# Optimization experiments

Measured on AMD Instinct MI355X. Metric: run time of the kernel, lower is better.

## Reference

```python
import jax, jax.numpy as jnp
import numpy as np

ENC_HID = 512
DEC_HID = 512


def setup_inputs() -> dict:
    key = jax.random.key(0)
    k1, k2, k3, k4, k5 = jax.random.split(key, 5)
    hidden = jax.random.normal(k1, (64, DEC_HID), dtype=jnp.float32)
    encoder_outputs = jax.random.normal(k2, (1024, 64, 2 * ENC_HID), dtype=jnp.float32)
    in_dim = 2 * ENC_HID + DEC_HID
    # Linear params (stored as [in, out] for x @ W + b)
    scale = 1.0 / np.sqrt(in_dim)
    W = jax.random.uniform(k3, (in_dim, DEC_HID), dtype=jnp.float32, minval=-scale, maxval=scale)
    b = jax.random.uniform(k4, (DEC_HID,), dtype=jnp.float32, minval=-scale, maxval=scale)
    v = jax.random.uniform(k5, (DEC_HID,), dtype=jnp.float32)  # torch.rand in [0,1)
    return {"hidden": hidden, "encoder_outputs": encoder_outputs, "W": W, "b": b, "v": v}


def reference(hidden, encoder_outputs, W, b, v):
    # hidden: [B, Dd]; encoder_outputs: [S, B, 2*De]
    src_len = encoder_outputs.shape[0]
    enc = jnp.transpose(encoder_outputs, (1, 0, 2))            # [B, S, 2*De]
    hid = jnp.broadcast_to(hidden[:, None, :], (hidden.shape[0], src_len, hidden.shape[1]))  # [B, S, Dd]
    concat = jnp.concatenate([hid, enc], axis=2)               # [B, S, Dd+2*De]
    energy = jnp.tanh(concat @ W + b)                          # [B, S, Dd]
    scores = jnp.einsum("bsd,d->bs", energy, v)                # [B, S]
    return jax.nn.softmax(scores, axis=1)
```

## Files before the change

### kernel.cpp

```cpp
#include <hip/hip_runtime.h>
#include <stdint.h>


typedef float  floatx4 __attribute__((ext_vector_type(4)));
typedef __bf16 bf16x8  __attribute__((ext_vector_type(8)));
typedef short  short8  __attribute__((ext_vector_type(8)));

union bfu { bf16x8 v; short8 s; };

#define LOG2E_X2 2.8853900817779268f

#define BAR()                                              \
  do {                                                     \
    asm volatile("s_waitcnt lgkmcnt(0)" ::: "memory");     \
    __builtin_amdgcn_sched_barrier(0);                     \
    __builtin_amdgcn_s_barrier();                          \
    __builtin_amdgcn_sched_barrier(0);                     \
  } while (0)

__global__ void wt_convert(const float* __restrict__ W, __bf16* __restrict__ Bp) {
  __shared__ float tile[64][65];
  const int kt = blockIdx.x >> 3;
  const int nt = blockIdx.x & 7;
  const int c  = threadIdx.x & 63;
  const int r4 = threadIdx.x >> 6;
  #pragma unroll 4
  for (int i = 0; i < 16; i++) {
    int r = i * 4 + r4;
    tile[r][c] = W[(long)(512 + kt * 64 + r) * 512 + nt * 64 + c];
  }
  __syncthreads();
  const int n_loc = threadIdx.x & 63;
  const int kc4   = threadIdx.x >> 6;
  const int n_g   = nt * 64 + n_loc;
  const int wv    = n_g >> 7;
  const int ct    = (n_g >> 4) & 7;
  const int t     = n_g & 15;
  #pragma unroll
  for (int i = 0; i < 2; i++) {
    int chunk = i * 4 + kc4;
    int k_g   = kt * 64 + chunk * 8;
    int T     = k_g >> 5;
    int q     = (k_g >> 3) & 3;
    union bfu u;
    #pragma unroll
    for (int j = 0; j < 8; j++) u.v[j] = (__bf16)tile[chunk * 8 + j][n_loc];
    long cidx = ((long)(T * 4 + wv) * 8 + ct) * 64 + q * 16 + t;
    *(bf16x8*)(Bp + cidx * 8) = u.v;
  }
}

__global__ void hproj_kernel(const float* __restrict__ hidden,
                             const float* __restrict__ W,
                             const float* __restrict__ bias,
                             float* __restrict__ hproj) {
  const int tid = threadIdx.x;
  const int b_  = blockIdx.x >> 2;
  const int kc  = blockIdx.x & 3;
  __shared__ float hid[128];
  if (tid < 128) hid[tid] = hidden[b_ * 512 + kc * 128 + tid];
  __syncthreads();
  float acc = (kc == 0) ? bias[tid] : 0.f;
  const float* Wp = W + (long)(kc * 128) * 512 + tid;
  #pragma unroll 8
  for (int k = 0; k < 128; k++) acc = fmaf(hid[k], Wp[(long)k * 512], acc);
  atomicAdd(&hproj[b_ * 512 + tid], acc);
}

__global__ __launch_bounds__(256, 2) void gemm_score(
    const float* __restrict__ enc,
    const __bf16* __restrict__ Bp,
    const float* __restrict__ hproj,
    const float* __restrict__ v,
    float* __restrict__ scores)
{
  __shared__ __bf16 ldsA[2][2048];
  __shared__ float bscore[64];

  const int tid  = threadIdx.x;
  const int lane = tid & 63;
  const int wv   = tid >> 6;
  const int q    = lane >> 4;
  const int t    = lane & 15;
  const long m0  = (long)blockIdx.x * 64;

  const int sm = tid >> 2;
  const int sf = tid & 3;
  const float* ap = enc + (m0 + sm) * 1024 + sf * 8;
  __bf16* aw0 = &ldsA[0][sf * 512 + ((sm * 8) ^ (sf * 16))];
  __bf16* aw1 = &ldsA[1][sf * 512 + ((sm * 8) ^ (sf * 16))];

  const __bf16* ar0 = &ldsA[0][q * 512 + ((t * 8) ^ (q * 16))];
  const __bf16* ar1 = &ldsA[1][q * 512 + ((t * 8) ^ (q * 16))];

  const __bf16* bpb = Bp + ((long)wv * 512 + lane) * 8;

  if (tid < 64) bscore[tid] = 0.f;

  floatx4 acc[4][8];
  #pragma unroll
  for (int i = 0; i < 4; i++)
    #pragma unroll
    for (int j = 0; j < 8; j++)
      acc[i][j] = (floatx4){0.f, 0.f, 0.f, 0.f};

  floatx4 ra[3][2];
  short8  bfr[2][8];

  auto issueA = [&](int T, int s) {
    const float* p = ap + T * 32;
    ra[s][0] = *(const floatx4*)(p);
    ra[s][1] = *(const floatx4*)(p + 4);
  };
  auto writeA = [&](int s, __bf16* dst) {
    union bfu u;
    #pragma unroll
    for (int j = 0; j < 4; j++) {
      u.v[j]     = (__bf16)ra[s][0][j];
      u.v[4 + j] = (__bf16)ra[s][1][j];
    }
    *(bf16x8*)dst = u.v;
  };
  auto loadB = [&](int T, int s) {
    #pragma unroll
    for (int ct = 0; ct < 8; ct++) {
      union bfu u;
      u.v = *(const bf16x8*)(bpb + (long)T * 16384 + ct * 512);
      bfr[s][ct] = u.s;
    }
  };
  auto compute = [&](const __bf16* base, int bs) {
    #pragma unroll
    for (int rt = 0; rt < 4; rt++) {
      union bfu u;
      u.v = *(const bf16x8*)(base + rt * 128);
      #pragma unroll
      for (int ct = 0; ct < 8; ct++)
        acc[rt][ct] = __builtin_amdgcn_mfma_f32_16x16x32_bf16(
            u.s, bfr[bs][ct], acc[rt][ct], 0, 0, 0);
    }
  };

  issueA(0, 0); issueA(1, 1); issueA(2, 2);
  loadB(0, 0);  loadB(1, 1);
  writeA(0, aw0);
  BAR();

#define PHASE(T, SI, SW)                                   \
  {                                                        \
    if ((T) < 29) issueA((T) + 3, SI);                     \
    if ((T) < 31) writeA(SW, ((T) & 1) ? aw0 : aw1);       \
    compute(((T) & 1) ? ar1 : ar0, (T) & 1);               \
    if ((T) < 30) loadB((T) + 2, (T) & 1);                 \
    BAR();                                                 \
  }

  PHASE(0, 0, 1)  PHASE(1, 1, 2)  PHASE(2, 2, 0)  PHASE(3, 0, 1)
  PHASE(4, 1, 2)  PHASE(5, 2, 0)  PHASE(6, 0, 1)  PHASE(7, 1, 2)
  PHASE(8, 2, 0)  PHASE(9, 0, 1)  PHASE(10, 1, 2) PHASE(11, 2, 0)
  PHASE(12, 0, 1) PHASE(13, 1, 2) PHASE(14, 2, 0) PHASE(15, 0, 1)
  PHASE(16, 1, 2) PHASE(17, 2, 0) PHASE(18, 0, 1) PHASE(19, 1, 2)
  PHASE(20, 2, 0) PHASE(21, 0, 1) PHASE(22, 1, 2) PHASE(23, 2, 0)
  PHASE(24, 0, 1) PHASE(25, 1, 2) PHASE(26, 2, 0) PHASE(27, 0, 1)
  PHASE(28, 1, 2) PHASE(29, 2, 0) PHASE(30, 0, 1) PHASE(31, 1, 2)
#undef PHASE

  float vv[8];
  #pragma unroll
  for (int ct = 0; ct < 8; ct++) vv[ct] = v[wv * 128 + ct * 16 + t];

  #pragma unroll
  for (int rt = 0; rt < 4; rt++) {
    #pragma unroll
    for (int r = 0; r < 4; r++) {
      int row = rt * 16 + q * 4 + r;
      const float* hrow = hproj + row * 512 + wv * 128 + t;
      float s = 0.f;
      #pragma unroll
      for (int ct = 0; ct < 8; ct++) {
        float e  = acc[rt][ct][r] + hrow[ct * 16];
        float ex = __builtin_amdgcn_exp2f(e * LOG2E_X2);
        float th = 1.f - 2.f * __builtin_amdgcn_rcpf(ex + 1.f);
        s = fmaf(vv[ct], th, s);
      }
      s += __shfl_xor(s, 1);
      s += __shfl_xor(s, 2);
      s += __shfl_xor(s, 4);
      s += __shfl_xor(s, 8);
      if (t == 0) atomicAdd(&bscore[row], s);
    }
  }
  __syncthreads();
  if (tid < 64) scores[(long)tid * 1024 + blockIdx.x] = bscore[tid];
}

__global__ void softmax_kernel(const float* __restrict__ scores,
                               float* __restrict__ out) {
  const int b_   = blockIdx.x;
  const int tid  = threadIdx.x;
  const int lane = tid & 63;
  const int wv   = tid >> 6;
  __shared__ float redmax[4], redsum[4];

  float x[4];
  #pragma unroll
  for (int i = 0; i < 4; i++) x[i] = scores[b_ * 1024 + i * 256 + tid];
  float mx = fmaxf(fmaxf(x[0], x[1]), fmaxf(x[2], x[3]));
  #pragma unroll
  for (int off = 1; off < 64; off <<= 1) mx = fmaxf(mx, __shfl_xor(mx, off));
  if (lane == 0) redmax[wv] = mx;
  __syncthreads();
  mx = fmaxf(fmaxf(redmax[0], redmax[1]), fmaxf(redmax[2], redmax[3]));

  float e[4], s = 0.f;
  #pragma unroll
  for (int i = 0; i < 4; i++) { e[i] = __expf(x[i] - mx); s += e[i]; }
  #pragma unroll
  for (int off = 1; off < 64; off <<= 1) s += __shfl_xor(s, off);
  if (lane == 0) redsum[wv] = s;
  __syncthreads();
  s = redsum[0] + redsum[1] + redsum[2] + redsum[3];
  float inv = 1.f / s;
  #pragma unroll
  for (int i = 0; i < 4; i++) out[b_ * 1024 + i * 256 + tid] = e[i] * inv;
}

extern "C" void kernel_launch(void* const* d_in, const int* in_sizes, int n_in,
                              void* d_out, int out_size, void* d_ws, size_t ws_size,
                              hipStream_t stream) {
  (void)in_sizes; (void)n_in; (void)out_size; (void)ws_size;
  const float* hidden = (const float*)d_in[0];
  const float* enc    = (const float*)d_in[1];
  const float* W      = (const float*)d_in[2];
  const float* bias   = (const float*)d_in[3];
  const float* v      = (const float*)d_in[4];
  float* out = (float*)d_out;

  char* ws = (char*)d_ws;
  __bf16* Bp    = (__bf16*)ws;
  float*  hproj = (float*)(ws + (1 << 20));
  float*  scores= (float*)(ws + (1 << 20) + (128 << 10));

  hipMemsetAsync(hproj, 0, 64 * 512 * sizeof(float), stream);
  wt_convert<<<128, 256, 0, stream>>>(W, Bp);
  hproj_kernel<<<256, 512, 0, stream>>>(hidden, W, bias, hproj);
  gemm_score<<<1024, 256, 0, stream>>>(enc, Bp, hproj, v, scores);
  softmax_kernel<<<64, 256, 0, stream>>>(scores, out);
}
```

Before: 417.3 us.

## Split gemm_score tile across 8 waves and reorder loads after MFMA compute

Doubles the gemm_score block to 512 threads with waves arranged as a 2x4 grid over rows and columns. Each wave now holds half the accumulators (2x8 tiles instead of 4x8), which frees registers and raises occupancy. Each thread loads one float4 of the A tile per phase instead of two. Each phase is reordered so the MFMA compute runs first, followed by the LDS write and B loads, with the next global A load issued last and sched_barriers fencing the groups. Every wave now reloads the full B fragments, doubling B traffic per block through L2/L1.

```diff
diff --git a/kernel.cpp b/kernel.cpp
--- a/kernel.cpp
+++ b/kernel.cpp
@@ -3,10 +3,12 @@
 
 
 typedef float  floatx4 __attribute__((ext_vector_type(4)));
+typedef __bf16 bf16x4  __attribute__((ext_vector_type(4)));
 typedef __bf16 bf16x8  __attribute__((ext_vector_type(8)));
 typedef short  short8  __attribute__((ext_vector_type(8)));
 
-union bfu { bf16x8 v; short8 s; };
+union bfu  { bf16x8 v; short8 s; };
+union bfu4 { bf16x4 v; uint2 u; };
 
 #define LOG2E_X2 2.8853900817779268f
 
@@ -17,6 +19,8 @@
     __builtin_amdgcn_s_barrier();                          \
     __builtin_amdgcn_sched_barrier(0);                     \
   } while (0)
+
+#define SB() __builtin_amdgcn_sched_barrier(0)
 
 __global__ void wt_convert(const float* __restrict__ W, __bf16* __restrict__ Bp) {
   __shared__ float tile[64][65];
@@ -33,7 +37,7 @@
   const int n_loc = threadIdx.x & 63;
   const int kc4   = threadIdx.x >> 6;
   const int n_g   = nt * 64 + n_loc;
-  const int wv    = n_g >> 7;
+  const int wc    = n_g >> 7;
   const int ct    = (n_g >> 4) & 7;
   const int t     = n_g & 15;
   #pragma unroll
@@ -45,7 +49,7 @@
     union bfu u;
     #pragma unroll
     for (int j = 0; j < 8; j++) u.v[j] = (__bf16)tile[chunk * 8 + j][n_loc];
-    long cidx = ((long)(T * 4 + wv) * 8 + ct) * 64 + q * 16 + t;
+    long cidx = ((long)(T * 4 + wc) * 8 + ct) * 64 + q * 16 + t;
     *(bf16x8*)(Bp + cidx * 8) = u.v;
   }
 }
@@ -67,7 +71,7 @@
   atomicAdd(&hproj[b_ * 512 + tid], acc);
 }
 
-__global__ __launch_bounds__(256, 2) void gemm_score(
+__global__ __launch_bounds__(512, 4) void gemm_score(
     const float* __restrict__ enc,
     const __bf16* __restrict__ Bp,
     const float* __restrict__ hproj,
@@ -80,46 +84,42 @@
   const int tid  = threadIdx.x;
   const int lane = tid & 63;
   const int wv   = tid >> 6;
+  const int wc   = wv & 3;
+  const int wr   = wv >> 2;
   const int q    = lane >> 4;
   const int t    = lane & 15;
   const long m0  = (long)blockIdx.x * 64;
 
-  const int sm = tid >> 2;
-  const int sf = tid & 3;
-  const float* ap = enc + (m0 + sm) * 1024 + sf * 8;
-  __bf16* aw0 = &ldsA[0][sf * 512 + ((sm * 8) ^ (sf * 16))];
-  __bf16* aw1 = &ldsA[1][sf * 512 + ((sm * 8) ^ (sf * 16))];
-
-  const __bf16* ar0 = &ldsA[0][q * 512 + ((t * 8) ^ (q * 16))];
-  const __bf16* ar1 = &ldsA[1][q * 512 + ((t * 8) ^ (q * 16))];
-
-  const __bf16* bpb = Bp + ((long)wv * 512 + lane) * 8;
+  const int m  = tid >> 3;
+  const int kq = tid & 7;
+  const float* ap = enc + (m0 + m) * 1024 + kq * 4;
+  const int c_  = kq >> 1;
+  const int jh  = (kq & 1) * 4;
+  __bf16* aw0 = &ldsA[0][c_ * 512 + ((m * 8) ^ (c_ * 16)) + jh];
+  __bf16* aw1 = &ldsA[1][c_ * 512 + ((m * 8) ^ (c_ * 16)) + jh];
+
+  const __bf16* ar0 = &ldsA[0][q * 512 + (((wr * 32 + t) * 8) ^ (q * 16))];
+  const __bf16* ar1 = &ldsA[1][q * 512 + (((wr * 32 + t) * 8) ^ (q * 16))];
+
+  const __bf16* bpb = Bp + ((long)wc * 512 + lane) * 8;
 
   if (tid < 64) bscore[tid] = 0.f;
 
-  floatx4 acc[4][8];
-  #pragma unroll
-  for (int i = 0; i < 4; i++)
+  floatx4 acc[2][8];
+  #pragma unroll
+  for (int i = 0; i < 2; i++)
     #pragma unroll
     for (int j = 0; j < 8; j++)
       acc[i][j] = (floatx4){0.f, 0.f, 0.f, 0.f};
 
-  floatx4 ra[3][2];
+  floatx4 ra0, ra1, ra2;
   short8  bfr[2][8];
 
-  auto issueA = [&](int T, int s) {
-    const float* p = ap + T * 32;
-    ra[s][0] = *(const floatx4*)(p);
-    ra[s][1] = *(const floatx4*)(p + 4);
-  };
-  auto writeA = [&](int s, __bf16* dst) {
-    union bfu u;
-    #pragma unroll
-    for (int j = 0; j < 4; j++) {
-      u.v[j]     = (__bf16)ra[s][0][j];
-      u.v[4 + j] = (__bf16)ra[s][1][j];
-    }
-    *(bf16x8*)dst = u.v;
+  auto writeA = [&](const floatx4& r, __bf16* dst) {
+    union bfu4 u;
+    #pragma unroll
+    for (int j = 0; j < 4; j++) u.v[j] = (__bf16)r[j];
+    *(bf16x4*)dst = u.v;
   };
   auto loadB = [&](int T, int s) {
     #pragma unroll
@@ -131,7 +131,7 @@
   };
   auto compute = [&](const __bf16* base, int bs) {
     #pragma unroll
-    for (int rt = 0; rt < 4; rt++) {
+    for (int rt = 0; rt < 2; rt++) {
       union bfu u;
       u.v = *(const bf16x8*)(base + rt * 128);
       #pragma unroll
@@ -141,40 +141,44 @@
     }
   };
 
-  issueA(0, 0); issueA(1, 1); issueA(2, 2);
+  ra0 = *(const floatx4*)(ap);
+  ra1 = *(const floatx4*)(ap + 32);
+  ra2 = *(const floatx4*)(ap + 64);
   loadB(0, 0);  loadB(1, 1);
-  writeA(0, aw0);
+  writeA(ra0, aw0);
   BAR();
 
-#define PHASE(T, SI, SW)                                   \
+#define PHASE(T, RI, RW)                                   \
   {                                                        \
-    if ((T) < 29) issueA((T) + 3, SI);                     \
-    if ((T) < 31) writeA(SW, ((T) & 1) ? aw0 : aw1);       \
     compute(((T) & 1) ? ar1 : ar0, (T) & 1);               \
+    SB();                                                  \
+    if ((T) < 31) writeA(RW, ((T) & 1) ? aw0 : aw1);       \
     if ((T) < 30) loadB((T) + 2, (T) & 1);                 \
+    SB();                                                  \
+    if ((T) < 29) RI = *(const floatx4*)(ap + ((T) + 3) * 32); \
     BAR();                                                 \
   }
 
-  PHASE(0, 0, 1)  PHASE(1, 1, 2)  PHASE(2, 2, 0)  PHASE(3, 0, 1)
-  PHASE(4, 1, 2)  PHASE(5, 2, 0)  PHASE(6, 0, 1)  PHASE(7, 1, 2)
-  PHASE(8, 2, 0)  PHASE(9, 0, 1)  PHASE(10, 1, 2) PHASE(11, 2, 0)
-  PHASE(12, 0, 1) PHASE(13, 1, 2) PHASE(14, 2, 0) PHASE(15, 0, 1)
-  PHASE(16, 1, 2) PHASE(17, 2, 0) PHASE(18, 0, 1) PHASE(19, 1, 2)
-  PHASE(20, 2, 0) PHASE(21, 0, 1) PHASE(22, 1, 2) PHASE(23, 2, 0)
-  PHASE(24, 0, 1) PHASE(25, 1, 2) PHASE(26, 2, 0) PHASE(27, 0, 1)
-  PHASE(28, 1, 2) PHASE(29, 2, 0) PHASE(30, 0, 1) PHASE(31, 1, 2)
+  PHASE(0, ra0, ra1)  PHASE(1, ra1, ra2)  PHASE(2, ra2, ra0)  PHASE(3, ra0, ra1)
+  PHASE(4, ra1, ra2)  PHASE(5, ra2, ra0)  PHASE(6, ra0, ra1)  PHASE(7, ra1, ra2)
+  PHASE(8, ra2, ra0)  PHASE(9, ra0, ra1)  PHASE(10, ra1, ra2) PHASE(11, ra2, ra0)
+  PHASE(12, ra0, ra1) PHASE(13, ra1, ra2) PHASE(14, ra2, ra0) PHASE(15, ra0, ra1)
+  PHASE(16, ra1, ra2) PHASE(17, ra2, ra0) PHASE(18, ra0, ra1) PHASE(19, ra1, ra2)
+  PHASE(20, ra2, ra0) PHASE(21, ra0, ra1) PHASE(22, ra1, ra2) PHASE(23, ra2, ra0)
+  PHASE(24, ra0, ra1) PHASE(25, ra1, ra2) PHASE(26, ra2, ra0) PHASE(27, ra0, ra1)
+  PHASE(28, ra1, ra2) PHASE(29, ra2, ra0) PHASE(30, ra0, ra1) PHASE(31, ra1, ra2)
 #undef PHASE
 
   float vv[8];
   #pragma unroll
-  for (int ct = 0; ct < 8; ct++) vv[ct] = v[wv * 128 + ct * 16 + t];
-
-  #pragma unroll
-  for (int rt = 0; rt < 4; rt++) {
+  for (int ct = 0; ct < 8; ct++) vv[ct] = v[wc * 128 + ct * 16 + t];
+
+  #pragma unroll
+  for (int rt = 0; rt < 2; rt++) {
     #pragma unroll
     for (int r = 0; r < 4; r++) {
-      int row = rt * 16 + q * 4 + r;
-      const float* hrow = hproj + row * 512 + wv * 128 + t;
+      int row = wr * 32 + rt * 16 + q * 4 + r;
+      const float* hrow = hproj + row * 512 + wc * 128 + t;
       float s = 0.f;
       #pragma unroll
       for (int ct = 0; ct < 8; ct++) {
@@ -244,6 +248,6 @@
   hipMemsetAsync(hproj, 0, 64 * 512 * sizeof(float), stream);
   wt_convert<<<128, 256, 0, stream>>>(W, Bp);
   hproj_kernel<<<256, 512, 0, stream>>>(hidden, W, bias, hproj);
-  gemm_score<<<1024, 256, 0, stream>>>(enc, Bp, hproj, v, scores);
+  gemm_score<<<1024, 512, 0, stream>>>(enc, Bp, hproj, v, scores);
   softmax_kernel<<<64, 256, 0, stream>>>(scores, out);
 }
```

Measured after the change: 1.125 ms. 2.7x slower.

## Double GEMM block tile to 128 rows with 8 waves sharing B fragments

Applied to the files above, without the earlier changes.

Each GEMM block now handles 128 rows with 512 threads arranged as 2 row-waves by 4 column-waves, so each B fragment load from global serves two waves' row tiles and the grid is halved. The per-phase order is also changed to run compute first, then the LDS write and B prefetch, then the next global A load, with scheduling barriers between them. This aims to cut redundant B-matrix traffic and improve latency hiding. The cost is larger LDS use and higher register pressure per block at 512 threads with two blocks per CU, which may reduce occupancy or cause spills.

```diff
diff --git a/kernel.cpp b/kernel.cpp
--- a/kernel.cpp
+++ b/kernel.cpp
@@ -6,7 +6,7 @@
 typedef __bf16 bf16x8  __attribute__((ext_vector_type(8)));
 typedef short  short8  __attribute__((ext_vector_type(8)));
 
-union bfu { bf16x8 v; short8 s; };
+union bfu  { bf16x8 v; short8 s; };
 
 #define LOG2E_X2 2.8853900817779268f
 
@@ -17,6 +17,8 @@
     __builtin_amdgcn_s_barrier();                          \
     __builtin_amdgcn_sched_barrier(0);                     \
   } while (0)
+
+#define SB() __builtin_amdgcn_sched_barrier(0)
 
 __global__ void wt_convert(const float* __restrict__ W, __bf16* __restrict__ Bp) {
   __shared__ float tile[64][65];
@@ -33,7 +35,7 @@
   const int n_loc = threadIdx.x & 63;
   const int kc4   = threadIdx.x >> 6;
   const int n_g   = nt * 64 + n_loc;
-  const int wv    = n_g >> 7;
+  const int wc    = n_g >> 7;
   const int ct    = (n_g >> 4) & 7;
   const int t     = n_g & 15;
   #pragma unroll
@@ -45,7 +47,7 @@
     union bfu u;
     #pragma unroll
     for (int j = 0; j < 8; j++) u.v[j] = (__bf16)tile[chunk * 8 + j][n_loc];
-    long cidx = ((long)(T * 4 + wv) * 8 + ct) * 64 + q * 16 + t;
+    long cidx = ((long)(T * 4 + wc) * 8 + ct) * 64 + q * 16 + t;
     *(bf16x8*)(Bp + cidx * 8) = u.v;
   }
 }
@@ -67,35 +69,37 @@
   atomicAdd(&hproj[b_ * 512 + tid], acc);
 }
 
-__global__ __launch_bounds__(256, 2) void gemm_score(
+__global__ __launch_bounds__(512, 2) void gemm_score(
     const float* __restrict__ enc,
     const __bf16* __restrict__ Bp,
     const float* __restrict__ hproj,
     const float* __restrict__ v,
     float* __restrict__ scores)
 {
-  __shared__ __bf16 ldsA[2][2048];
-  __shared__ float bscore[64];
+  __shared__ __bf16 ldsA[2][4096];
+  __shared__ float bscore[128];
 
   const int tid  = threadIdx.x;
   const int lane = tid & 63;
   const int wv   = tid >> 6;
+  const int wc   = wv & 3;
+  const int wr   = wv >> 2;
   const int q    = lane >> 4;
   const int t    = lane & 15;
-  const long m0  = (long)blockIdx.x * 64;
+  const long m0  = (long)blockIdx.x * 128;
 
   const int sm = tid >> 2;
   const int sf = tid & 3;
   const float* ap = enc + (m0 + sm) * 1024 + sf * 8;
-  __bf16* aw0 = &ldsA[0][sf * 512 + ((sm * 8) ^ (sf * 16))];
-  __bf16* aw1 = &ldsA[1][sf * 512 + ((sm * 8) ^ (sf * 16))];
-
-  const __bf16* ar0 = &ldsA[0][q * 512 + ((t * 8) ^ (q * 16))];
-  const __bf16* ar1 = &ldsA[1][q * 512 + ((t * 8) ^ (q * 16))];
-
-  const __bf16* bpb = Bp + ((long)wv * 512 + lane) * 8;
-
-  if (tid < 64) bscore[tid] = 0.f;
+  __bf16* aw0 = &ldsA[0][sf * 1024 + ((sm * 8) ^ (sf * 16))];
+  __bf16* aw1 = &ldsA[1][sf * 1024 + ((sm * 8) ^ (sf * 16))];
+
+  const __bf16* ar0 = &ldsA[0][q * 1024 + wr * 512 + ((t * 8) ^ (q * 16))];
+  const __bf16* ar1 = &ldsA[1][q * 1024 + wr * 512 + ((t * 8) ^ (q * 16))];
+
+  const __bf16* bpb = Bp + (long)wc * 4096 + (long)lane * 8;
+
+  if (tid < 128) bscore[tid] = 0.f;
 
   floatx4 acc[4][8];
   #pragma unroll
@@ -146,35 +150,37 @@
   writeA(0, aw0);
   BAR();
 
-#define PHASE(T, SI, SW)                                   \
+#define PHASE(T)                                           \
   {                                                        \
-    if ((T) < 29) issueA((T) + 3, SI);                     \
-    if ((T) < 31) writeA(SW, ((T) & 1) ? aw0 : aw1);       \
     compute(((T) & 1) ? ar1 : ar0, (T) & 1);               \
+    SB();                                                  \
+    if ((T) < 31) writeA(((T) + 1) % 3, ((T) & 1) ? aw0 : aw1); \
     if ((T) < 30) loadB((T) + 2, (T) & 1);                 \
+    SB();                                                  \
+    if ((T) < 29) issueA((T) + 3, (T) % 3);                \
     BAR();                                                 \
   }
 
-  PHASE(0, 0, 1)  PHASE(1, 1, 2)  PHASE(2, 2, 0)  PHASE(3, 0, 1)
-  PHASE(4, 1, 2)  PHASE(5, 2, 0)  PHASE(6, 0, 1)  PHASE(7, 1, 2)
-  PHASE(8, 2, 0)  PHASE(9, 0, 1)  PHASE(10, 1, 2) PHASE(11, 2, 0)
-  PHASE(12, 0, 1) PHASE(13, 1, 2) PHASE(14, 2, 0) PHASE(15, 0, 1)
-  PHASE(16, 1, 2) PHASE(17, 2, 0) PHASE(18, 0, 1) PHASE(19, 1, 2)
-  PHASE(20, 2, 0) PHASE(21, 0, 1) PHASE(22, 1, 2) PHASE(23, 2, 0)
-  PHASE(24, 0, 1) PHASE(25, 1, 2) PHASE(26, 2, 0) PHASE(27, 0, 1)
-  PHASE(28, 1, 2) PHASE(29, 2, 0) PHASE(30, 0, 1) PHASE(31, 1, 2)
+  PHASE(0)  PHASE(1)  PHASE(2)  PHASE(3)
+  PHASE(4)  PHASE(5)  PHASE(6)  PHASE(7)
+  PHASE(8)  PHASE(9)  PHASE(10) PHASE(11)
+  PHASE(12) PHASE(13) PHASE(14) PHASE(15)
+  PHASE(16) PHASE(17) PHASE(18) PHASE(19)
+  PHASE(20) PHASE(21) PHASE(22) PHASE(23)
+  PHASE(24) PHASE(25) PHASE(26) PHASE(27)
+  PHASE(28) PHASE(29) PHASE(30) PHASE(31)
 #undef PHASE
 
   float vv[8];
   #pragma unroll
-  for (int ct = 0; ct < 8; ct++) vv[ct] = v[wv * 128 + ct * 16 + t];
+  for (int ct = 0; ct < 8; ct++) vv[ct] = v[wc * 128 + ct * 16 + t];
 
   #pragma unroll
   for (int rt = 0; rt < 4; rt++) {
     #pragma unroll
     for (int r = 0; r < 4; r++) {
-      int row = rt * 16 + q * 4 + r;
-      const float* hrow = hproj + row * 512 + wv * 128 + t;
+      int row = wr * 64 + rt * 16 + q * 4 + r;
+      const float* hrow = hproj + (row & 63) * 512 + wc * 128 + t;
       float s = 0.f;
       #pragma unroll
       for (int ct = 0; ct < 8; ct++) {
@@ -191,7 +197,8 @@
     }
   }
   __syncthreads();
-  if (tid < 64) scores[(long)tid * 1024 + blockIdx.x] = bscore[tid];
+  if (tid < 128)
+    scores[(long)(tid & 63) * 1024 + blockIdx.x * 2 + (tid >> 6)] = bscore[tid];
 }
 
 __global__ void softmax_kernel(const float* __restrict__ scores,
@@ -244,6 +251,6 @@
   hipMemsetAsync(hproj, 0, 64 * 512 * sizeof(float), stream);
   wt_convert<<<128, 256, 0, stream>>>(W, Bp);
   hproj_kernel<<<256, 512, 0, stream>>>(hidden, W, bias, hproj);
-  gemm_score<<<1024, 256, 0, stream>>>(enc, Bp, hproj, v, scores);
+  gemm_score<<<512, 512, 0, stream>>>(enc, Bp, hproj, v, scores);
   softmax_kernel<<<64, 256, 0, stream>>>(scores, out);
 }
```

After: 430.2 us. 1.03x slower.
